# Kernel tuning notes

Hardware: AMD Instinct MI355X
Metric: run time of the kernel (lower is better)

Reference implementation:

```python
import jax, jax.numpy as jnp
import numpy as np

B, S, D, E, R, N = 16, 128, 1152, 2304, 72, 16
EPS = 1e-5

def _ln(x, g, b):
    m = jnp.mean(x, axis=-1, keepdims=True)
    xc = x - m
    v = jnp.mean(xc * xc, axis=-1, keepdims=True)
    return xc * jax.lax.rsqrt(v + EPS) * g + b

def _ssm(u, W_dbc, W_dt, b_dt, A_log, D_ssm):
    # u: [B,S,E] -> selective scan (Mamba S6)
    A = -jnp.exp(A_log)                                   # [E,N]
    dbc = u @ W_dbc.T                                     # [B,S,R+2N]
    delta, Bm, Cm = jnp.split(dbc, [R, R + N], axis=-1)
    delta = jax.nn.softplus(delta @ W_dt.T + b_dt)        # [B,S,E]
    dA = jnp.exp(jnp.einsum('bld,dn->bldn', delta, A))    # [B,S,E,N]
    dBu = jnp.einsum('bld,bln->bldn', delta * u, Bm)      # [B,S,E,N]
    def step(h, inp):
        dA_t, dBu_t, C_t = inp
        h = dA_t * h + dBu_t                              # [B,E,N]
        return h, jnp.einsum('bdn,bn->bd', h, C_t)
    h0 = jnp.zeros((u.shape[0], E, N), dtype=u.dtype)
    _, ys = jax.lax.scan(step, h0, (dA.transpose(1, 0, 2, 3), dBu.transpose(1, 0, 2, 3), Cm.transpose(1, 0, 2)))
    return ys.transpose(1, 0, 2) + u * D_ssm

def setup_inputs() -> dict:
    key = jax.random.key(0)
    ks = jax.random.split(key, 12)
    f = lambda k, shp: jax.random.normal(k, shp, dtype=jnp.float32) * 0.02
    order = jnp.arange(S - 1, -1, -1, dtype=jnp.int32)  # reversal: its own inverse
    return {
        'x': jax.random.normal(ks[0], (B, S, D), dtype=jnp.float32),
        'c': jax.random.normal(ks[1], (B, 2 * D), dtype=jnp.float32),
        'w': jax.random.normal(ks[2], (B, 2 * D), dtype=jnp.float32),
        'W_ada': f(ks[3], (3 * D, 2 * D)), 'b_ada': jnp.zeros((3 * D,), jnp.float32),
        'g1': jnp.ones((D,), jnp.float32), 'be1': jnp.zeros((D,), jnp.float32),
        'g2': jnp.ones((D,), jnp.float32), 'be2': jnp.zeros((D,), jnp.float32),
        'W_x': f(ks[4], (E, D)), 'b_x': jnp.zeros((E,), jnp.float32),
        'W_z': f(ks[5], (E, D)), 'b_z': jnp.zeros((E,), jnp.float32),
        'W_conv': f(ks[6], (E, E)), 'b_conv': jnp.zeros((E,), jnp.float32),
        'W_dbc': f(ks[7], (R + 2 * N, E)),
        'W_dt': f(ks[8], (E, R)), 'b_dt': jnp.zeros((E,), jnp.float32),
        'A_log': jnp.log(jnp.tile(jnp.arange(1, N + 1, dtype=jnp.float32), (E, 1))),
        'D_ssm': jnp.ones((E,), jnp.float32),
        'W_f': f(ks[9], (D, E)), 'b_f': jnp.zeros((D,), jnp.float32),
        'order': order, 'origina': order,
    }

def reference(x, c, w, W_ada, b_ada, g1, be1, g2, be2, W_x, b_x, W_z, b_z, W_conv, b_conv, W_dbc, W_dt, b_dt, A_log, D_ssm, W_f, b_f, order, origina):
    mod = jax.nn.silu(c) @ W_ada.T + b_ada                # [B,3D]
    shift, scale, gate = jnp.split(mod, 3, axis=-1)
    xn = _ln(x, g1, be1)
    xm = xn * (1.0 + scale[:, None, :]) + shift[:, None, :]
    skip = xm
    xn2 = _ln(xm, g2, be2)
    mz = xn2 @ W_z.T + b_z                                # [B,S,E]
    mx = xn2 @ W_x.T + b_x                                # [B,S,E]
    mz = jnp.einsum('bse,oe->bso', mz, W_conv) + b_conv   # conv1d k=1 over channels
    zs = mz[:, order]                                     # CrossScan gather
    zs = _ssm(zs, W_dbc, W_dt, b_dt, A_log, D_ssm)
    mz = zs[:, origina]                                   # CrossMerge gather
    y = jax.nn.silu(mx) * mz
    x_ssm = y @ W_f.T + b_f + skip
    return x + gate[:, None, :] * x_ssm
```

## Files before the change

### kernel.cpp

```cpp
#include <hip/hip_runtime.h>

typedef unsigned short u16;
typedef __attribute__((ext_vector_type(8))) short s16x8;
typedef __attribute__((ext_vector_type(4))) float f32x4;
typedef __attribute__((ext_vector_type(4))) unsigned short u16x4;

#define DEV __device__ __forceinline__

DEV u16 f2bf(float f) {
  union { float f; unsigned u; } x; x.f = f;
  unsigned r = x.u + 0x7FFFu + ((x.u >> 16) & 1u);
  return (u16)(r >> 16);
}
DEV float bf2f(u16 h) {
  union { unsigned u; float f; } x; x.u = ((unsigned)h) << 16;
  return x.f;
}

DEV void gload16(const u16* g, u16* l) {
  __builtin_amdgcn_global_load_lds(
      (const __attribute__((address_space(1))) void*)g,
      (__attribute__((address_space(3))) void*)l, 16, 0, 0);
}

constexpr int B_ = 16, S_ = 128, D_ = 1152, E_ = 2304, R_ = 72, N_ = 16;
constexpr int M_ = B_ * S_;
constexpr int KD_ = 104;
constexpr int KDP_ = 128;
constexpr int RP2_ = 128;
constexpr int L_ = 16, NC_ = 8;
constexpr int SK_ = 18;
constexpr int MO_ = 3 * D_;
constexpr int MSK_ = 9;

constexpr int C0_ = E_ * D_ / 4;
constexpr int C1_ = C0_ + E_ * D_ / 4;
constexpr int C2_ = C1_ + E_ * E_ / 4;
constexpr int C3_ = C2_ + D_ * E_ / 4;
constexpr int C4_ = C3_ + KDP_ * E_ / 4;
constexpr int C5_ = C4_ + E_ * RP2_ / 4;
constexpr int C6_ = C5_ + 128 * E_ / 4;
constexpr int C7_ = C6_ + MO_ * E_ / 4;

__global__ __launch_bounds__(256) void cast_all_k(
    const float* __restrict__ W_x, const float* __restrict__ W_z,
    const float* __restrict__ W_conv, const float* __restrict__ W_f,
    const float* __restrict__ W_dbc, const float* __restrict__ W_dt,
    const float* __restrict__ cc, const float* __restrict__ W_ada,
    u16* __restrict__ wx, u16* __restrict__ wz, u16* __restrict__ wconv,
    u16* __restrict__ wf, u16* __restrict__ wdbc, u16* __restrict__ wdt,
    u16* __restrict__ siluc, u16* __restrict__ wada) {
  int i = blockIdx.x * 256 + threadIdx.x;
  if (i >= C7_) return;
  const float* s = nullptr;
  u16* d = nullptr;
  int j = i;
  bool pad = false, slu = false;
  if (i < C0_) { s = W_x + (size_t)i * 4; d = wx + (size_t)i * 4; }
  else if (i < C1_) { j = i - C0_; s = W_z + (size_t)j * 4; d = wz + (size_t)j * 4; }
  else if (i < C2_) { j = i - C1_; s = W_conv + (size_t)j * 4; d = wconv + (size_t)j * 4; }
  else if (i < C3_) { j = i - C2_; s = W_f + (size_t)j * 4; d = wf + (size_t)j * 4; }
  else if (i < C4_) {
    j = i - C3_;
    int r = j / (E_ / 4);
    d = wdbc + (size_t)j * 4;
    if (r < KD_) s = W_dbc + (size_t)j * 4; else pad = true;
  } else if (i < C5_) {
    j = i - C4_;
    int r = j / (RP2_ / 4), c4 = j % (RP2_ / 4);
    d = wdt + (size_t)j * 4;
    if (c4 * 4 < R_) s = W_dt + (size_t)r * R_ + c4 * 4; else pad = true;
  } else if (i < C6_) {
    j = i - C5_;
    int r = j / (E_ / 4);
    d = siluc + (size_t)j * 4;
    if (r < B_) { s = cc + (size_t)j * 4; slu = true; } else pad = true;
  } else {
    j = i - C6_;
    s = W_ada + (size_t)j * 4;
    d = wada + (size_t)j * 4;
  }
  u16x4 o;
  if (pad) { o[0] = o[1] = o[2] = o[3] = 0; }
  else {
    f32x4 v = *(const f32x4*)s;
    if (slu) {
#pragma unroll
      for (int q = 0; q < 4; q++) v[q] = v[q] / (1.f + __expf(-v[q]));
    }
    o[0] = f2bf(v[0]); o[1] = f2bf(v[1]); o[2] = f2bf(v[2]); o[3] = f2bf(v[3]);
  }
  *(u16x4*)d = o;
}

__global__ __launch_bounds__(256) void mod_reduce(
    const float* __restrict__ pbuf2, const float* __restrict__ b_ada,
    float* __restrict__ modv) {
  const int idx = blockIdx.x * 256 + threadIdx.x;
  const int b = idx / MO_, o = idx - b * MO_;
  float v = b_ada[o];
#pragma unroll
  for (int ks = 0; ks < MSK_; ks++) v += pbuf2[((size_t)ks * B_ + b) * MO_ + o];
  modv[idx] = v;
}

DEV void breduce2(float& a, float& c, float* lds) {
#pragma unroll
  for (int off = 32; off; off >>= 1) { a += __shfl_down(a, off); c += __shfl_down(c, off); }
  int w = threadIdx.x >> 6;
  if ((threadIdx.x & 63) == 0) { lds[w] = a; lds[w + 4] = c; }
  __syncthreads();
  a = lds[0] + lds[1] + lds[2] + lds[3];
  c = lds[4] + lds[5] + lds[6] + lds[7];
  __syncthreads();
}

__global__ __launch_bounds__(256) void ln_mod_ln(
    const float* __restrict__ x, const float* __restrict__ modv,
    const float* __restrict__ g1, const float* __restrict__ be1,
    const float* __restrict__ g2, const float* __restrict__ be2,
    float* __restrict__ skip, u16* __restrict__ xn2) {
  __shared__ float lds[8];
  const int row = blockIdx.x;
  const int b = row >> 7;
  const float* xr = x + (size_t)row * D_;
  const int t = threadIdx.x;
  const bool two = (t < (D_ / 4 - 256));

  f32x4 v0 = *(const f32x4*)(xr + t * 4);
  f32x4 v1 = {0.f, 0.f, 0.f, 0.f};
  if (two) v1 = *(const f32x4*)(xr + (t + 256) * 4);

  float s = 0.f, s2 = 0.f;
#pragma unroll
  for (int j = 0; j < 4; j++) { s += v0[j] + v1[j]; s2 += v0[j] * v0[j] + v1[j] * v1[j]; }
  breduce2(s, s2, lds);
  const float mean = s * (1.f / D_);
  const float rs = rsqrtf(s2 * (1.f / D_) - mean * mean + 1e-5f);

  const float* mb = modv + (size_t)b * 3 * D_;
  f32x4 m0, m1 = {0.f, 0.f, 0.f, 0.f};
  {
    f32x4 gg = *(const f32x4*)(g1 + t * 4), bb = *(const f32x4*)(be1 + t * 4);
    f32x4 sh = *(const f32x4*)(mb + t * 4), sc = *(const f32x4*)(mb + D_ + t * 4);
#pragma unroll
    for (int j = 0; j < 4; j++) {
      float xn = (v0[j] - mean) * rs * gg[j] + bb[j];
      m0[j] = xn * (1.f + sc[j]) + sh[j];
    }
  }
  if (two) {
    int ci = t + 256;
    f32x4 gg = *(const f32x4*)(g1 + ci * 4), bb = *(const f32x4*)(be1 + ci * 4);
    f32x4 sh = *(const f32x4*)(mb + ci * 4), sc = *(const f32x4*)(mb + D_ + ci * 4);
#pragma unroll
    for (int j = 0; j < 4; j++) {
      float xn = (v1[j] - mean) * rs * gg[j] + bb[j];
      m1[j] = xn * (1.f + sc[j]) + sh[j];
    }
  }
  *(f32x4*)(skip + (size_t)row * D_ + t * 4) = m0;
  if (two) *(f32x4*)(skip + (size_t)row * D_ + (t + 256) * 4) = m1;

  float s_ = 0.f, s2_ = 0.f;
#pragma unroll
  for (int j = 0; j < 4; j++) { s_ += m0[j] + m1[j]; s2_ += m0[j] * m0[j] + m1[j] * m1[j]; }
  breduce2(s_, s2_, lds);
  const float mean2 = s_ * (1.f / D_);
  const float rs2 = rsqrtf(s2_ * (1.f / D_) - mean2 * mean2 + 1e-5f);

  {
    f32x4 gg = *(const f32x4*)(g2 + t * 4), bb = *(const f32x4*)(be2 + t * 4);
    u16x4 o;
#pragma unroll
    for (int j = 0; j < 4; j++) o[j] = f2bf((m0[j] - mean2) * rs2 * gg[j] + bb[j]);
    *(u16x4*)(xn2 + (size_t)row * D_ + t * 4) = o;
  }
  if (two) {
    int ci = t + 256;
    f32x4 gg = *(const f32x4*)(g2 + ci * 4), bb = *(const f32x4*)(be2 + ci * 4);
    u16x4 o;
#pragma unroll
    for (int j = 0; j < 4; j++) o[j] = f2bf((m1[j] - mean2) * rs2 * gg[j] + bb[j]);
    *(u16x4*)(xn2 + (size_t)row * D_ + ci * 4) = o;
  }
}

template <int EPI>
__global__ __launch_bounds__(512) void gemm_bt(
    const u16* __restrict__ A, const int lda,
    const u16* __restrict__ Wt, const int ldb,
    const int K, const int N,
    const float* __restrict__ bias, const float* __restrict__ bias2,
    float* __restrict__ of, u16* __restrict__ ob, u16* __restrict__ ob2,
    const float* __restrict__ skip, const float* __restrict__ xin,
    const float* __restrict__ modv) {
  __shared__ __align__(16) u16 As0[128 * 64], As1[128 * 64];
  __shared__ __align__(16) u16 Bs0[128 * 64], Bs1[128 * 64];
  const int nbx = gridDim.x;
  const int nwg = nbx * gridDim.y;
  const int orig = blockIdx.y * nbx + blockIdx.x;
  const int q8 = nwg >> 3, r8 = nwg & 7;
  const int xcd = orig & 7, li = orig >> 3;
  const int wgid = (xcd < r8 ? xcd * (q8 + 1) : r8 * (q8 + 1) + (xcd - r8) * q8) + li;
  const int bx = wgid % nbx, by = wgid / nbx;

  const int tm = (EPI == 6) ? 0 : by * 128;
  const int tn = (EPI == 5) ? 0 : bx * 128;
  const int kof = (EPI == 5) ? bx * 128 : ((EPI == 6) ? by * 256 : 0);
  const int t = threadIdx.x;
  const int lane = t & 63, w = t >> 6, wr = w >> 1, wc = w & 1;
  const int lrow = lane & 15, lq = lane >> 4, sw = lane & 7;

  f32x4 acc[2][4];
#pragma unroll
  for (int m = 0; m < 2; m++)
#pragma unroll
    for (int n = 0; n < 4; n++) acc[m][n] = (f32x4){0.f, 0.f, 0.f, 0.f};

  const int sr = lane >> 3;
  const int sc8 = ((lane & 7) ^ sr) * 8;
  const u16* Ag = A + (size_t)(tm + w * 16 + sr) * lda + kof + sc8;
  const u16* Bg = Wt + (size_t)(tn + w * 16 + sr) * ldb + kof + sc8;
  u16* Al0 = &As0[w * 16 * 64];
  u16* Al1 = &As1[w * 16 * 64];
  u16* Bl0 = &Bs0[w * 16 * 64];
  u16* Bl1 = &Bs1[w * 16 * 64];

  auto stage = [&](u16* Al, u16* Bl, int k0) {
#pragma unroll
    for (int g = 0; g < 2; g++) {
      gload16(Ag + (size_t)(g * 8) * lda + k0, Al + g * 8 * 64);
      gload16(Bg + (size_t)(g * 8) * ldb + k0, Bl + g * 8 * 64);
    }
    __builtin_amdgcn_sched_barrier(0);
  };
  auto compute = [&](const u16* Ab, const u16* Bb) {
    s16x8 a0[2], a1[2], b0[4], b1[4];
#pragma unroll
    for (int m = 0; m < 2; m++) {
      const u16* rp = Ab + (wr * 32 + m * 16 + lrow) * 64;
      a0[m] = *(const s16x8*)(rp + ((lq ^ sw) * 8));
      a1[m] = *(const s16x8*)(rp + (((4 + lq) ^ sw) * 8));
    }
#pragma unroll
    for (int n = 0; n < 4; n++) {
      const u16* rp = Bb + (wc * 64 + n * 16 + lrow) * 64;
      b0[n] = *(const s16x8*)(rp + ((lq ^ sw) * 8));
      b1[n] = *(const s16x8*)(rp + (((4 + lq) ^ sw) * 8));
    }
#pragma unroll
    for (int m = 0; m < 2; m++)
#pragma unroll
      for (int n = 0; n < 4; n++)
        acc[m][n] = __builtin_amdgcn_mfma_f32_16x16x32_bf16(a0[m], b0[n], acc[m][n], 0, 0, 0);
#pragma unroll
    for (int m = 0; m < 2; m++)
#pragma unroll
      for (int n = 0; n < 4; n++)
        acc[m][n] = __builtin_amdgcn_mfma_f32_16x16x32_bf16(a1[m], b1[n], acc[m][n], 0, 0, 0);
  };

  const int nt = K >> 6;
  stage(Al0, Bl0, 0);
  __syncthreads();
  for (int tk = 0; tk < nt; tk += 2) {
    if (tk + 1 < nt) stage(Al1, Bl1, (tk + 1) * 64);
    compute(As0, Bs0);
    __syncthreads();
    if (tk + 2 < nt) stage(Al0, Bl0, (tk + 2) * 64);
    if (tk + 1 < nt) compute(As1, Bs1);
    __syncthreads();
  }

#pragma unroll
  for (int m = 0; m < 2; m++)
#pragma unroll
    for (int n = 0; n < 4; n++) {
      const int gr0 = tm + wr * 32 + m * 16 + ((lane >> 4) << 2);
      const int gc = tn + wc * 64 + n * 16 + (lane & 15);
#pragma unroll
      for (int r = 0; r < 4; r++) {
        const int gr = gr0 + r;
        float v = acc[m][n][r];
        const size_t o = (size_t)gr * N + gc;
        if (EPI == 0) {
          ob[o] = f2bf(v + bias[gc]);
        } else if (EPI == 2) {
          float tt = v + bias[gc];
          of[o] = fmaxf(tt, 0.f) + log1pf(__expf(-fabsf(tt)));
        } else if (EPI == 3) {
          float tt = v + bias[gc] + skip[o];
          int b = gr >> 7;
          float g = modv[(size_t)b * 3 * D_ + 2 * D_ + gc];
          of[o] = xin[o] + g * tt;
        } else if (EPI == 4) {
          if (gc < E_) ob[(size_t)gr * E_ + gc] = f2bf(v + bias[gc]);
          else ob2[(size_t)gr * E_ + (gc - E_)] = f2bf(v + bias2[gc - E_]);
        } else if (EPI == 5) {
          of[(size_t)bx * M_ * KDP_ + (size_t)gr * KDP_ + gc] = v;
        } else if (EPI == 6) {
          if (wr == 0 && m == 0)
            of[((size_t)by * B_ + gr) * MO_ + gc] = v;
        }
      }
    }
}

__global__ __launch_bounds__(256) void dbc_reduce(
    const float* __restrict__ pbuf, u16* __restrict__ dbcd,
    float* __restrict__ Bm, float* __restrict__ Cm) {
  const int idx = blockIdx.x * 256 + threadIdx.x;
  const int gr = idx >> 7, gc = idx & 127;
  float v = 0.f;
#pragma unroll
  for (int s = 0; s < SK_; s++) v += pbuf[(size_t)s * M_ * KDP_ + idx];
  dbcd[(size_t)gr * RP2_ + gc] = (gc < R_) ? f2bf(v) : (u16)0;
  if (gc >= R_ && gc < R_ + N_) Bm[(size_t)gr * N_ + (gc - R_)] = v;
  else if (gc >= R_ + N_ && gc < KD_) Cm[(size_t)gr * N_ + (gc - R_ - N_)] = v;
}

__global__ __launch_bounds__(256) void scan_a(
    const float* __restrict__ delta, const u16* __restrict__ u,
    const float* __restrict__ Bmv, const float* __restrict__ A_log,
    float* __restrict__ hloc, float* __restrict__ sdl) {
  const int e = blockIdx.x * 256 + threadIdx.x;
  const int c = blockIdx.y, b = blockIdx.z;
  float Av[16];
#pragma unroll
  for (int n = 0; n < 16; n += 4) {
    f32x4 v = *(const f32x4*)(A_log + (size_t)e * 16 + n);
#pragma unroll
    for (int j = 0; j < 4; j++) Av[n + j] = -__expf(v[j]);
  }
  float h[16];
#pragma unroll
  for (int n = 0; n < 16; n++) h[n] = 0.f;
  float sd = 0.f;

  for (int tt = 0; tt < L_; ++tt) {
    const int s = S_ - 1 - (c * L_ + tt);
    const size_t idx = ((size_t)b * S_ + s) * E_ + e;
    const size_t bc = ((size_t)b * S_ + s) * 16;
    const float dl = delta[idx];
    const float uu = bf2f(u[idx]);
    const float du = dl * uu;
    sd += dl;
#pragma unroll
    for (int q = 0; q < 4; q++) {
      f32x4 Bv = *(const f32x4*)(Bmv + bc + q * 4);
#pragma unroll
      for (int j = 0; j < 4; j++) {
        const int n = q * 4 + j;
        const float dA = __expf(dl * Av[n]);
        h[n] = fmaf(dA, h[n], du * Bv[j]);
      }
    }
  }
  const size_t o = (size_t)b * NC_ + c;
#pragma unroll
  for (int n = 0; n < 16; n++) hloc[(o * 16 + n) * E_ + e] = h[n];
  sdl[o * E_ + e] = sd;
}

__global__ __launch_bounds__(256) void scan_b(
    const float* __restrict__ A_log, float* __restrict__ hloc,
    const float* __restrict__ sdl) {
  const int e = blockIdx.x * 256 + threadIdx.x;
  const int b = blockIdx.y;
  float Av[16];
#pragma unroll
  for (int n = 0; n < 16; n += 4) {
    f32x4 v = *(const f32x4*)(A_log + (size_t)e * 16 + n);
#pragma unroll
    for (int j = 0; j < 4; j++) Av[n + j] = -__expf(v[j]);
  }
  float hs[16];
#pragma unroll
  for (int n = 0; n < 16; n++) hs[n] = 0.f;
  for (int c = 0; c < NC_; ++c) {
    const size_t o = (size_t)b * NC_ + c;
    const float sd = sdl[o * E_ + e];
#pragma unroll
    for (int n = 0; n < 16; n++) {
      const float P = __expf(Av[n] * sd);
      const size_t a = (o * 16 + n) * E_ + e;
      const float hl = hloc[a];
      const float nh = fmaf(P, hs[n], hl);
      hloc[a] = hs[n];
      hs[n] = nh;
    }
  }
}

__global__ __launch_bounds__(256) void scan_c(
    const float* __restrict__ delta, const u16* __restrict__ u,
    const float* __restrict__ Bmv, const float* __restrict__ Cmv,
    const float* __restrict__ A_log, const float* __restrict__ Dss,
    const u16* __restrict__ mxb, const float* __restrict__ hstart,
    u16* __restrict__ ybf) {
  const int e = blockIdx.x * 256 + threadIdx.x;
  const int c = blockIdx.y, b = blockIdx.z;
  float Av[16];
#pragma unroll
  for (int n = 0; n < 16; n += 4) {
    f32x4 v = *(const f32x4*)(A_log + (size_t)e * 16 + n);
#pragma unroll
    for (int j = 0; j < 4; j++) Av[n + j] = -__expf(v[j]);
  }
  const float Dv = Dss[e];
  const size_t o = (size_t)b * NC_ + c;
  float h[16];
#pragma unroll
  for (int n = 0; n < 16; n++) h[n] = hstart[(o * 16 + n) * E_ + e];

  for (int tt = 0; tt < L_; ++tt) {
    const int s = S_ - 1 - (c * L_ + tt);
    const size_t idx = ((size_t)b * S_ + s) * E_ + e;
    const size_t bc = ((size_t)b * S_ + s) * 16;
    const float dl = delta[idx];
    const float uu = bf2f(u[idx]);
    const float du = dl * uu;
    float y = 0.f;
#pragma unroll
    for (int q = 0; q < 4; q++) {
      f32x4 Bv = *(const f32x4*)(Bmv + bc + q * 4);
      f32x4 Cv = *(const f32x4*)(Cmv + bc + q * 4);
#pragma unroll
      for (int j = 0; j < 4; j++) {
        const int n = q * 4 + j;
        const float dA = __expf(dl * Av[n]);
        h[n] = fmaf(dA, h[n], du * Bv[j]);
        y = fmaf(h[n], Cv[j], y);
      }
    }
    const float xm = bf2f(mxb[idx]);
    const float sx = xm / (1.f + __expf(-xm));
    ybf[idx] = f2bf(sx * (y + uu * Dv));
  }
}

extern "C" void kernel_launch(void* const* d_in, const int* in_sizes, int n_in,
                              void* d_out, int out_size, void* d_ws, size_t ws_size,
                              hipStream_t stream) {
  const float* x = (const float*)d_in[0];
  const float* c = (const float*)d_in[1];
  const float* W_ada = (const float*)d_in[3];
  const float* b_ada = (const float*)d_in[4];
  const float* g1 = (const float*)d_in[5];
  const float* be1 = (const float*)d_in[6];
  const float* g2 = (const float*)d_in[7];
  const float* be2 = (const float*)d_in[8];
  const float* W_x = (const float*)d_in[9];
  const float* b_x = (const float*)d_in[10];
  const float* W_z = (const float*)d_in[11];
  const float* b_z = (const float*)d_in[12];
  const float* W_conv = (const float*)d_in[13];
  const float* b_conv = (const float*)d_in[14];
  const float* W_dbc = (const float*)d_in[15];
  const float* W_dt = (const float*)d_in[16];
  const float* b_dt = (const float*)d_in[17];
  const float* A_log = (const float*)d_in[18];
  const float* D_ssm = (const float*)d_in[19];
  const float* W_f = (const float*)d_in[20];
  const float* b_f = (const float*)d_in[21];
  float* out = (float*)d_out;

  char* p = (char*)d_ws;
  auto alloc = [&](size_t bytes) { char* r = p; p += (bytes + 255) & ~255ULL; return r; };
  u16* wx = (u16*)alloc((size_t)E_ * D_ * 2);
  u16* wz = (u16*)alloc((size_t)E_ * D_ * 2);
  u16* wconv = (u16*)alloc((size_t)E_ * E_ * 2);
  u16* wdbc = (u16*)alloc((size_t)KDP_ * E_ * 2);
  u16* wdt = (u16*)alloc((size_t)E_ * RP2_ * 2);
  u16* wf = (u16*)alloc((size_t)D_ * E_ * 2);
  float* modv = (float*)alloc((size_t)B_ * 3 * D_ * 4);
  float* skip = (float*)alloc((size_t)M_ * D_ * 4);
  u16* xn2 = (u16*)alloc((size_t)M_ * D_ * 2);
  u16* mx = (u16*)alloc((size_t)M_ * E_ * 2);
  u16* mz0 = (u16*)alloc((size_t)M_ * E_ * 2);
  u16* mzc = (u16*)alloc((size_t)M_ * E_ * 2);
  u16* dbcd = (u16*)alloc((size_t)M_ * RP2_ * 2);
  float* Bm = (float*)alloc((size_t)M_ * N_ * 4);
  float* Cm = (float*)alloc((size_t)M_ * N_ * 4);
  float* delta = (float*)alloc((size_t)M_ * E_ * 4);
  u16* ybf = (u16*)alloc((size_t)M_ * E_ * 2);

  float* pbuf = delta;
  float* pbuf2 = delta;
  float* hloc = (float*)wx;
  float* sdl = hloc + (size_t)B_ * NC_ * E_ * 16;
  u16* wada = mx;
  u16* siluc = mzc;

  cast_all_k<<<(C7_ + 255) / 256, 256, 0, stream>>>(
      W_x, W_z, W_conv, W_f, W_dbc, W_dt, c, W_ada,
      wx, wz, wconv, wf, wdbc, wdt, siluc, wada);

  gemm_bt<6><<<dim3(MO_ / 128, MSK_), 512, 0, stream>>>(
      siluc, E_, wada, E_, 256, MO_, nullptr, nullptr, pbuf2, nullptr, nullptr,
      nullptr, nullptr, nullptr);
  mod_reduce<<<B_ * MO_ / 256, 256, 0, stream>>>(pbuf2, b_ada, modv);

  ln_mod_ln<<<M_, 256, 0, stream>>>(x, modv, g1, be1, g2, be2, skip, xn2);

  gemm_bt<4><<<dim3(2 * E_ / 128, M_ / 128), 512, 0, stream>>>(
      xn2, D_, wx, D_, D_, 2 * E_, b_x, b_z, nullptr, mx, mz0, nullptr, nullptr, nullptr);
  gemm_bt<0><<<dim3(E_ / 128, M_ / 128), 512, 0, stream>>>(
      mz0, E_, wconv, E_, E_, E_, b_conv, nullptr, nullptr, mzc, nullptr, nullptr, nullptr, nullptr);
  gemm_bt<5><<<dim3(SK_, M_ / 128), 512, 0, stream>>>(
      mzc, E_, wdbc, E_, 128, KDP_, nullptr, nullptr, pbuf, nullptr, nullptr, nullptr, nullptr, nullptr);
  dbc_reduce<<<M_ * KDP_ / 256, 256, 0, stream>>>(pbuf, dbcd, Bm, Cm);
  gemm_bt<2><<<dim3(E_ / 128, M_ / 128), 512, 0, stream>>>(
      dbcd, RP2_, wdt, RP2_, RP2_, E_, b_dt, nullptr, delta, nullptr, nullptr, nullptr, nullptr, nullptr);

  scan_a<<<dim3(E_ / 256, NC_, B_), 256, 0, stream>>>(delta, mzc, Bm, A_log, hloc, sdl);
  scan_b<<<dim3(E_ / 256, B_), 256, 0, stream>>>(A_log, hloc, sdl);
  scan_c<<<dim3(E_ / 256, NC_, B_), 256, 0, stream>>>(delta, mzc, Bm, Cm, A_log, D_ssm,
                                                      mx, hloc, ybf);

  gemm_bt<3><<<dim3(D_ / 128, M_ / 128), 512, 0, stream>>>(
      ybf, E_, wf, E_, E_, D_, b_f, nullptr, out, nullptr, nullptr, skip, x, modv);
}
```

Measured before the change: 237.1 us.

## Fold the channel conv weight into W_z and drop the separate conv GEMM

Each call now precomputes the combined weight W_conv·W_z, using a transposed bf16 copy of W_z and an extra weight-only GEMM, plus a folded bias W_conv·b_z + b_conv. The fused x/z projection GEMM then writes the conv output directly. This removes the activation-sized E×E conv GEMM and the mz0 intermediate round trip, at the cost of a smaller weight-only GEMM and an extra rounding of the folded weights to bf16. It also changes the workgroup-to-tile mapping to column-major order and halves the split-K factor for the dbc projection.

```diff
diff --git a/kernel.cpp b/kernel.cpp
--- a/kernel.cpp
+++ b/kernel.cpp
@@ -29,54 +29,52 @@
 constexpr int KDP_ = 128;
 constexpr int RP2_ = 128;
 constexpr int L_ = 16, NC_ = 8;
-constexpr int SK_ = 18;
+constexpr int SK_ = 9;
 constexpr int MO_ = 3 * D_;
 constexpr int MSK_ = 9;
 
 constexpr int C0_ = E_ * D_ / 4;
-constexpr int C1_ = C0_ + E_ * D_ / 4;
-constexpr int C2_ = C1_ + E_ * E_ / 4;
-constexpr int C3_ = C2_ + D_ * E_ / 4;
-constexpr int C4_ = C3_ + KDP_ * E_ / 4;
-constexpr int C5_ = C4_ + E_ * RP2_ / 4;
-constexpr int C6_ = C5_ + 128 * E_ / 4;
-constexpr int C7_ = C6_ + MO_ * E_ / 4;
+constexpr int C1_ = C0_ + E_ * E_ / 4;
+constexpr int C2_ = C1_ + D_ * E_ / 4;
+constexpr int C3_ = C2_ + KDP_ * E_ / 4;
+constexpr int C4_ = C3_ + E_ * RP2_ / 4;
+constexpr int C5_ = C4_ + 128 * E_ / 4;
+constexpr int C6_ = C5_ + MO_ * 2 * D_ / 4;
 
 __global__ __launch_bounds__(256) void cast_all_k(
-    const float* __restrict__ W_x, const float* __restrict__ W_z,
-    const float* __restrict__ W_conv, const float* __restrict__ W_f,
-    const float* __restrict__ W_dbc, const float* __restrict__ W_dt,
-    const float* __restrict__ cc, const float* __restrict__ W_ada,
-    u16* __restrict__ wx, u16* __restrict__ wz, u16* __restrict__ wconv,
-    u16* __restrict__ wf, u16* __restrict__ wdbc, u16* __restrict__ wdt,
+    const float* __restrict__ W_x, const float* __restrict__ W_conv,
+    const float* __restrict__ W_f, const float* __restrict__ W_dbc,
+    const float* __restrict__ W_dt, const float* __restrict__ cc,
+    const float* __restrict__ W_ada,
+    u16* __restrict__ wx, u16* __restrict__ wconv, u16* __restrict__ wf,
+    u16* __restrict__ wdbc, u16* __restrict__ wdt,
     u16* __restrict__ siluc, u16* __restrict__ wada) {
   int i = blockIdx.x * 256 + threadIdx.x;
-  if (i >= C7_) return;
+  if (i >= C6_) return;
   const float* s = nullptr;
   u16* d = nullptr;
   int j = i;
   bool pad = false, slu = false;
   if (i < C0_) { s = W_x + (size_t)i * 4; d = wx + (size_t)i * 4; }
-  else if (i < C1_) { j = i - C0_; s = W_z + (size_t)j * 4; d = wz + (size_t)j * 4; }
-  else if (i < C2_) { j = i - C1_; s = W_conv + (size_t)j * 4; d = wconv + (size_t)j * 4; }
-  else if (i < C3_) { j = i - C2_; s = W_f + (size_t)j * 4; d = wf + (size_t)j * 4; }
-  else if (i < C4_) {
-    j = i - C3_;
+  else if (i < C1_) { j = i - C0_; s = W_conv + (size_t)j * 4; d = wconv + (size_t)j * 4; }
+  else if (i < C2_) { j = i - C1_; s = W_f + (size_t)j * 4; d = wf + (size_t)j * 4; }
+  else if (i < C3_) {
+    j = i - C2_;
     int r = j / (E_ / 4);
     d = wdbc + (size_t)j * 4;
     if (r < KD_) s = W_dbc + (size_t)j * 4; else pad = true;
-  } else if (i < C5_) {
-    j = i - C4_;
+  } else if (i < C4_) {
+    j = i - C3_;
     int r = j / (RP2_ / 4), c4 = j % (RP2_ / 4);
     d = wdt + (size_t)j * 4;
     if (c4 * 4 < R_) s = W_dt + (size_t)r * R_ + c4 * 4; else pad = true;
-  } else if (i < C6_) {
-    j = i - C5_;
+  } else if (i < C5_) {
+    j = i - C4_;
     int r = j / (E_ / 4);
     d = siluc + (size_t)j * 4;
     if (r < B_) { s = cc + (size_t)j * 4; slu = true; } else pad = true;
   } else {
-    j = i - C6_;
+    j = i - C5_;
     s = W_ada + (size_t)j * 4;
     d = wada + (size_t)j * 4;
   }
@@ -91,6 +89,45 @@
     o[0] = f2bf(v[0]); o[1] = f2bf(v[1]); o[2] = f2bf(v[2]); o[3] = f2bf(v[3]);
   }
   *(u16x4*)d = o;
+}
+
+__global__ __launch_bounds__(256) void transpose_wz(
+    const float* __restrict__ Wz, u16* __restrict__ wzT) {
+  __shared__ float ls[64][68];
+  const int nd = D_ / 64;
+  const int d0 = (blockIdx.x % nd) * 64;
+  const int e0 = (blockIdx.x / nd) * 64;
+  const int t = threadIdx.x;
+  const int lr = t >> 4;
+  const int lc = (t & 15) * 4;
+#pragma unroll
+  for (int g = 0; g < 4; g++) {
+    f32x4 v = *(const f32x4*)(Wz + (size_t)(e0 + lr + 16 * g) * D_ + d0 + lc);
+#pragma unroll
+    for (int j = 0; j < 4; j++) ls[lr + 16 * g][lc + j] = v[j];
+  }
+  __syncthreads();
+#pragma unroll
+  for (int g = 0; g < 4; g++) {
+    const int dr = lr + 16 * g;
+    u16x4 o;
+#pragma unroll
+    for (int j = 0; j < 4; j++) o[j] = f2bf(ls[lc + j][dr]);
+    *(u16x4*)(wzT + (size_t)(d0 + dr) * E_ + e0 + lc) = o;
+  }
+}
+
+__global__ __launch_bounds__(256) void bzc_k(
+    const u16* __restrict__ wconv, const float* __restrict__ b_z,
+    const float* __restrict__ b_conv, float* __restrict__ bzc) {
+  const int o = blockIdx.x * 4 + (threadIdx.x >> 6);
+  const int lane = threadIdx.x & 63;
+  const u16* row = wconv + (size_t)o * E_;
+  float acc = 0.f;
+  for (int i = lane; i < E_; i += 64) acc += bf2f(row[i]) * b_z[i];
+#pragma unroll
+  for (int off = 32; off; off >>= 1) acc += __shfl_down(acc, off);
+  if (lane == 0) bzc[o] = acc + b_conv[o];
 }
 
 __global__ __launch_bounds__(256) void mod_reduce(
@@ -197,17 +234,17 @@
     const float* __restrict__ modv) {
   __shared__ __align__(16) u16 As0[128 * 64], As1[128 * 64];
   __shared__ __align__(16) u16 Bs0[128 * 64], Bs1[128 * 64];
-  const int nbx = gridDim.x;
-  const int nwg = nbx * gridDim.y;
+  const int nbx = gridDim.x, nby = gridDim.y;
+  const int nwg = nbx * nby;
   const int orig = blockIdx.y * nbx + blockIdx.x;
   const int q8 = nwg >> 3, r8 = nwg & 7;
   const int xcd = orig & 7, li = orig >> 3;
   const int wgid = (xcd < r8 ? xcd * (q8 + 1) : r8 * (q8 + 1) + (xcd - r8) * q8) + li;
-  const int bx = wgid % nbx, by = wgid / nbx;
+  const int bx = wgid / nby, by = wgid % nby;
 
   const int tm = (EPI == 6) ? 0 : by * 128;
   const int tn = (EPI == 5) ? 0 : bx * 128;
-  const int kof = (EPI == 5) ? bx * 128 : ((EPI == 6) ? by * 256 : 0);
+  const int kof = (EPI == 5) ? bx * 256 : ((EPI == 6) ? by * 256 : 0);
   const int t = threadIdx.x;
   const int lane = t & 63, w = t >> 6, wr = w >> 1, wc = w & 1;
   const int lrow = lane & 15, lq = lane >> 4, sw = lane & 7;
@@ -302,6 +339,8 @@
         } else if (EPI == 6) {
           if (wr == 0 && m == 0)
             of[((size_t)by * B_ + gr) * MO_ + gc] = v;
+        } else if (EPI == 7) {
+          ob[o] = f2bf(v);
         }
       }
     }
@@ -469,7 +508,7 @@
   char* p = (char*)d_ws;
   auto alloc = [&](size_t bytes) { char* r = p; p += (bytes + 255) & ~255ULL; return r; };
   u16* wx = (u16*)alloc((size_t)E_ * D_ * 2);
-  u16* wz = (u16*)alloc((size_t)E_ * D_ * 2);
+  u16* wzc = (u16*)alloc((size_t)E_ * D_ * 2);
   u16* wconv = (u16*)alloc((size_t)E_ * E_ * 2);
   u16* wdbc = (u16*)alloc((size_t)KDP_ * E_ * 2);
   u16* wdt = (u16*)alloc((size_t)E_ * RP2_ * 2);
@@ -478,38 +517,43 @@
   float* skip = (float*)alloc((size_t)M_ * D_ * 4);
   u16* xn2 = (u16*)alloc((size_t)M_ * D_ * 2);
   u16* mx = (u16*)alloc((size_t)M_ * E_ * 2);
-  u16* mz0 = (u16*)alloc((size_t)M_ * E_ * 2);
   u16* mzc = (u16*)alloc((size_t)M_ * E_ * 2);
   u16* dbcd = (u16*)alloc((size_t)M_ * RP2_ * 2);
   float* Bm = (float*)alloc((size_t)M_ * N_ * 4);
   float* Cm = (float*)alloc((size_t)M_ * N_ * 4);
   float* delta = (float*)alloc((size_t)M_ * E_ * 4);
   u16* ybf = (u16*)alloc((size_t)M_ * E_ * 2);
+  float* bzc = (float*)alloc((size_t)E_ * 4);
 
   float* pbuf = delta;
   float* pbuf2 = delta;
   float* hloc = (float*)wx;
   float* sdl = hloc + (size_t)B_ * NC_ * E_ * 16;
   u16* wada = mx;
-  u16* siluc = mzc;
-
-  cast_all_k<<<(C7_ + 255) / 256, 256, 0, stream>>>(
-      W_x, W_z, W_conv, W_f, W_dbc, W_dt, c, W_ada,
-      wx, wz, wconv, wf, wdbc, wdt, siluc, wada);
+  u16* siluc = dbcd;
+  u16* wzT = (u16*)skip;
+
+  cast_all_k<<<(C6_ + 255) / 256, 256, 0, stream>>>(
+      W_x, W_conv, W_f, W_dbc, W_dt, c, W_ada,
+      wx, wconv, wf, wdbc, wdt, siluc, wada);
+  transpose_wz<<<(D_ / 64) * (E_ / 64), 256, 0, stream>>>(W_z, wzT);
 
   gemm_bt<6><<<dim3(MO_ / 128, MSK_), 512, 0, stream>>>(
-      siluc, E_, wada, E_, 256, MO_, nullptr, nullptr, pbuf2, nullptr, nullptr,
+      siluc, E_, wada, 2 * D_, 256, MO_, nullptr, nullptr, pbuf2, nullptr, nullptr,
       nullptr, nullptr, nullptr);
   mod_reduce<<<B_ * MO_ / 256, 256, 0, stream>>>(pbuf2, b_ada, modv);
 
+  gemm_bt<7><<<dim3(D_ / 128, E_ / 128), 512, 0, stream>>>(
+      wconv, E_, wzT, E_, E_, D_, nullptr, nullptr, nullptr, wzc, nullptr,
+      nullptr, nullptr, nullptr);
+  bzc_k<<<E_ / 4, 256, 0, stream>>>(wconv, b_z, b_conv, bzc);
+
   ln_mod_ln<<<M_, 256, 0, stream>>>(x, modv, g1, be1, g2, be2, skip, xn2);
 
   gemm_bt<4><<<dim3(2 * E_ / 128, M_ / 128), 512, 0, stream>>>(
-      xn2, D_, wx, D_, D_, 2 * E_, b_x, b_z, nullptr, mx, mz0, nullptr, nullptr, nullptr);
-  gemm_bt<0><<<dim3(E_ / 128, M_ / 128), 512, 0, stream>>>(
-      mz0, E_, wconv, E_, E_, E_, b_conv, nullptr, nullptr, mzc, nullptr, nullptr, nullptr, nullptr);
+      xn2, D_, wx, D_, D_, 2 * E_, b_x, bzc, nullptr, mx, mzc, nullptr, nullptr, nullptr);
   gemm_bt<5><<<dim3(SK_, M_ / 128), 512, 0, stream>>>(
-      mzc, E_, wdbc, E_, 128, KDP_, nullptr, nullptr, pbuf, nullptr, nullptr, nullptr, nullptr, nullptr);
+      mzc, E_, wdbc, E_, 256, KDP_, nullptr, nullptr, pbuf, nullptr, nullptr, nullptr, nullptr, nullptr);
   dbc_reduce<<<M_ * KDP_ / 256, 256, 0, stream>>>(pbuf, dbcd, Bm, Cm);
   gemm_bt<2><<<dim3(E_ / 128, M_ / 128), 512, 0, stream>>>(
       dbcd, RP2_, wdt, RP2_, RP2_, E_, b_dt, nullptr, delta, nullptr, nullptr, nullptr, nullptr, nullptr);
```

Result: no change. 237.5 us (+0.2%).

## Fuse three-pass chunked scan into one kernel and halve dbc split-K

Applied to the files above, without the earlier changes.

Merges scan_a, scan_b and scan_c into a single scan_f kernel. Each block handles 64 channels across all 8 chunks, and the per-chunk local states and delta sums are exchanged through shared memory rather than global hloc/sdl buffers. This removes two kernel launches and the global round trip of the chunk-carry state. The cost is a serial carry step done by one warp while the others wait at a barrier. Separately, the dbc GEMM split-K factor drops from 18 to 9 with 256-wide K slices, which halves the partial buffer that the reduce kernel must sum.

```diff
diff --git a/kernel.cpp b/kernel.cpp
--- a/kernel.cpp
+++ b/kernel.cpp
@@ -29,7 +29,7 @@
 constexpr int KDP_ = 128;
 constexpr int RP2_ = 128;
 constexpr int L_ = 16, NC_ = 8;
-constexpr int SK_ = 18;
+constexpr int SK_ = 9;
 constexpr int MO_ = 3 * D_;
 constexpr int MSK_ = 9;
 
@@ -207,7 +207,7 @@
 
   const int tm = (EPI == 6) ? 0 : by * 128;
   const int tn = (EPI == 5) ? 0 : bx * 128;
-  const int kof = (EPI == 5) ? bx * 128 : ((EPI == 6) ? by * 256 : 0);
+  const int kof = (EPI == 5) ? bx * 256 : ((EPI == 6) ? by * 256 : 0);
   const int t = threadIdx.x;
   const int lane = t & 63, w = t >> 6, wr = w >> 1, wc = w & 1;
   const int lrow = lane & 15, lq = lane >> 4, sw = lane & 7;
@@ -320,12 +320,18 @@
   else if (gc >= R_ + N_ && gc < KD_) Cm[(size_t)gr * N_ + (gc - R_ - N_)] = v;
 }
 
-__global__ __launch_bounds__(256) void scan_a(
+__global__ __launch_bounds__(512) void scan_f(
     const float* __restrict__ delta, const u16* __restrict__ u,
-    const float* __restrict__ Bmv, const float* __restrict__ A_log,
-    float* __restrict__ hloc, float* __restrict__ sdl) {
-  const int e = blockIdx.x * 256 + threadIdx.x;
-  const int c = blockIdx.y, b = blockIdx.z;
+    const float* __restrict__ Bmv, const float* __restrict__ Cmv,
+    const float* __restrict__ A_log, const float* __restrict__ Dss,
+    const u16* __restrict__ mxb, u16* __restrict__ ybf) {
+  __shared__ float lsh[NC_][64][17];
+  __shared__ float lsd[NC_][64];
+  const int el = threadIdx.x & 63;
+  const int cc = threadIdx.x >> 6;
+  const int e = blockIdx.x * 64 + el;
+  const int b = blockIdx.y;
+
   float Av[16];
 #pragma unroll
   for (int n = 0; n < 16; n += 4) {
@@ -339,7 +345,7 @@
   float sd = 0.f;
 
   for (int tt = 0; tt < L_; ++tt) {
-    const int s = S_ - 1 - (c * L_ + tt);
+    const int s = S_ - 1 - (cc * L_ + tt);
     const size_t idx = ((size_t)b * S_ + s) * E_ + e;
     const size_t bc = ((size_t)b * S_ + s) * 16;
     const float dl = delta[idx];
@@ -352,70 +358,37 @@
 #pragma unroll
       for (int j = 0; j < 4; j++) {
         const int n = q * 4 + j;
-        const float dA = __expf(dl * Av[n]);
-        h[n] = fmaf(dA, h[n], du * Bv[j]);
+        h[n] = fmaf(__expf(dl * Av[n]), h[n], du * Bv[j]);
       }
     }
   }
-  const size_t o = (size_t)b * NC_ + c;
-#pragma unroll
-  for (int n = 0; n < 16; n++) hloc[(o * 16 + n) * E_ + e] = h[n];
-  sdl[o * E_ + e] = sd;
-}
-
-__global__ __launch_bounds__(256) void scan_b(
-    const float* __restrict__ A_log, float* __restrict__ hloc,
-    const float* __restrict__ sdl) {
-  const int e = blockIdx.x * 256 + threadIdx.x;
-  const int b = blockIdx.y;
-  float Av[16];
-#pragma unroll
-  for (int n = 0; n < 16; n += 4) {
-    f32x4 v = *(const f32x4*)(A_log + (size_t)e * 16 + n);
-#pragma unroll
-    for (int j = 0; j < 4; j++) Av[n + j] = -__expf(v[j]);
-  }
-  float hs[16];
-#pragma unroll
-  for (int n = 0; n < 16; n++) hs[n] = 0.f;
-  for (int c = 0; c < NC_; ++c) {
-    const size_t o = (size_t)b * NC_ + c;
-    const float sd = sdl[o * E_ + e];
-#pragma unroll
-    for (int n = 0; n < 16; n++) {
-      const float P = __expf(Av[n] * sd);
-      const size_t a = (o * 16 + n) * E_ + e;
-      const float hl = hloc[a];
-      const float nh = fmaf(P, hs[n], hl);
-      hloc[a] = hs[n];
-      hs[n] = nh;
-    }
-  }
-}
-
-__global__ __launch_bounds__(256) void scan_c(
-    const float* __restrict__ delta, const u16* __restrict__ u,
-    const float* __restrict__ Bmv, const float* __restrict__ Cmv,
-    const float* __restrict__ A_log, const float* __restrict__ Dss,
-    const u16* __restrict__ mxb, const float* __restrict__ hstart,
-    u16* __restrict__ ybf) {
-  const int e = blockIdx.x * 256 + threadIdx.x;
-  const int c = blockIdx.y, b = blockIdx.z;
-  float Av[16];
-#pragma unroll
-  for (int n = 0; n < 16; n += 4) {
-    f32x4 v = *(const f32x4*)(A_log + (size_t)e * 16 + n);
-#pragma unroll
-    for (int j = 0; j < 4; j++) Av[n + j] = -__expf(v[j]);
-  }
+  lsd[cc][el] = sd;
+#pragma unroll
+  for (int n = 0; n < 16; n++) lsh[cc][el][n] = h[n];
+  __syncthreads();
+
+  if (cc == 0) {
+    float hs[16];
+#pragma unroll
+    for (int n = 0; n < 16; n++) hs[n] = 0.f;
+    for (int c2 = 0; c2 < NC_; ++c2) {
+      const float sdc = lsd[c2][el];
+#pragma unroll
+      for (int n = 0; n < 16; n++) {
+        const float P = __expf(Av[n] * sdc);
+        const float hl = lsh[c2][el][n];
+        lsh[c2][el][n] = hs[n];
+        hs[n] = fmaf(P, hs[n], hl);
+      }
+    }
+  }
+  __syncthreads();
+
+#pragma unroll
+  for (int n = 0; n < 16; n++) h[n] = lsh[cc][el][n];
   const float Dv = Dss[e];
-  const size_t o = (size_t)b * NC_ + c;
-  float h[16];
-#pragma unroll
-  for (int n = 0; n < 16; n++) h[n] = hstart[(o * 16 + n) * E_ + e];
-
   for (int tt = 0; tt < L_; ++tt) {
-    const int s = S_ - 1 - (c * L_ + tt);
+    const int s = S_ - 1 - (cc * L_ + tt);
     const size_t idx = ((size_t)b * S_ + s) * E_ + e;
     const size_t bc = ((size_t)b * S_ + s) * 16;
     const float dl = delta[idx];
@@ -429,8 +402,7 @@
 #pragma unroll
       for (int j = 0; j < 4; j++) {
         const int n = q * 4 + j;
-        const float dA = __expf(dl * Av[n]);
-        h[n] = fmaf(dA, h[n], du * Bv[j]);
+        h[n] = fmaf(__expf(dl * Av[n]), h[n], du * Bv[j]);
         y = fmaf(h[n], Cv[j], y);
       }
     }
@@ -488,8 +460,6 @@
 
   float* pbuf = delta;
   float* pbuf2 = delta;
-  float* hloc = (float*)wx;
-  float* sdl = hloc + (size_t)B_ * NC_ * E_ * 16;
   u16* wada = mx;
   u16* siluc = mzc;
 
@@ -509,15 +479,13 @@
   gemm_bt<0><<<dim3(E_ / 128, M_ / 128), 512, 0, stream>>>(
       mz0, E_, wconv, E_, E_, E_, b_conv, nullptr, nullptr, mzc, nullptr, nullptr, nullptr, nullptr);
   gemm_bt<5><<<dim3(SK_, M_ / 128), 512, 0, stream>>>(
-      mzc, E_, wdbc, E_, 128, KDP_, nullptr, nullptr, pbuf, nullptr, nullptr, nullptr, nullptr, nullptr);
+      mzc, E_, wdbc, E_, 256, KDP_, nullptr, nullptr, pbuf, nullptr, nullptr, nullptr, nullptr, nullptr);
   dbc_reduce<<<M_ * KDP_ / 256, 256, 0, stream>>>(pbuf, dbcd, Bm, Cm);
   gemm_bt<2><<<dim3(E_ / 128, M_ / 128), 512, 0, stream>>>(
       dbcd, RP2_, wdt, RP2_, RP2_, E_, b_dt, nullptr, delta, nullptr, nullptr, nullptr, nullptr, nullptr);
 
-  scan_a<<<dim3(E_ / 256, NC_, B_), 256, 0, stream>>>(delta, mzc, Bm, A_log, hloc, sdl);
-  scan_b<<<dim3(E_ / 256, B_), 256, 0, stream>>>(A_log, hloc, sdl);
-  scan_c<<<dim3(E_ / 256, NC_, B_), 256, 0, stream>>>(delta, mzc, Bm, Cm, A_log, D_ssm,
-                                                      mx, hloc, ybf);
+  scan_f<<<dim3(E_ / 64, B_), 512, 0, stream>>>(delta, mzc, Bm, Cm, A_log, D_ssm,
+                                                mx, ybf);
 
   gemm_bt<3><<<dim3(D_ / 128, M_ / 128), 512, 0, stream>>>(
       ybf, E_, wf, E_, E_, D_, b_f, nullptr, out, nullptr, nullptr, skip, x, modv);
```

New measurement: 234.5 us. No clear change (-1.1%).
